# Optimization experiments

Measured on AMD Instinct MI355X. Metric: run time of the kernel, lower is better.

The kernel has to match this reference:

```python
import jax, jax.numpy as jnp
import numpy as np

H = 1024          # hidden_dim
E = 8             # num_experts
TOP_K = 2
FF = 4 * H        # ExpertFFN inner dim (standard transformer FFN assumption)
B, S = 2, 2048


def setup_inputs() -> dict:
    key = jax.random.key(0)
    ks = jax.random.split(key, 12)
    std = 0.02 / np.sqrt(H)
    return {
        "x": jax.random.normal(ks[0], (B, S, H), dtype=jnp.float32),
        "gate_w": jax.random.normal(ks[1], (E, H), dtype=jnp.float32) * std,  # nn.Linear weight [out,in]
        "gate_b": jnp.zeros((E,), dtype=jnp.float32),                          # self.bias param
        # routed experts, stacked: FFN = W2 @ gelu(W1 @ x + b1) + b2
        "w1": jax.random.normal(ks[2], (E, H, FF), dtype=jnp.float32) * (1.0 / np.sqrt(H)),
        "b1": jnp.zeros((E, FF), dtype=jnp.float32),
        "w2": jax.random.normal(ks[3], (E, FF, H), dtype=jnp.float32) * (1.0 / np.sqrt(FF)),
        "b2": jnp.zeros((E, H), dtype=jnp.float32),
        # shared expert
        "sw1": jax.random.normal(ks[4], (H, FF), dtype=jnp.float32) * (1.0 / np.sqrt(H)),
        "sb1": jnp.zeros((FF,), dtype=jnp.float32),
        "sw2": jax.random.normal(ks[5], (FF, H), dtype=jnp.float32) * (1.0 / np.sqrt(FF)),
        "sb2": jnp.zeros((H,), dtype=jnp.float32),
    }


def _moe_forward(x, gate_w, gate_b, w1, b1, w2, b2, sw1, sb1, sw2, sb2):
    b, s, h = x.shape
    xf = x.reshape(-1, h)                                    # [T, H]
    # sigmoid gating with learned bias (aux-loss-free load balancing bias)
    scores = jax.nn.sigmoid(xf @ gate_w.T + gate_b)          # [T, E]
    top_scores, top_idx = jax.lax.top_k(scores, TOP_K)       # [T, k]
    top_scores = top_scores / (top_scores.sum(-1, keepdims=True) + 1e-6)
    # per-expert combine weights: sum of normalized scores over top-k slots
    comb = (jax.nn.one_hot(top_idx, E, dtype=xf.dtype) * top_scores[..., None]).sum(1)  # [T, E]
    # dense grouped FFN over all experts (reference; faithful math to masked dispatch)
    hdn = jax.nn.gelu(jnp.einsum('th,ehf->etf', xf, w1) + b1[:, None, :], approximate=False)
    y = jnp.einsum('etf,efh->eth', hdn, w2) + b2[:, None, :]  # [E, T, H]
    routed = jnp.einsum('te,eth->th', comb, y)                # [T, H]
    shared = (jax.nn.gelu(xf @ sw1 + sb1, approximate=False) @ sw2 + sb2) * 0.1
    return (routed + shared).reshape(b, s, h)                 # dropout: eval mode (identity)


def reference(x, gate_w, gate_b, w1, b1, w2, b2, sw1, sb1, sw2, sb2):
    return _moe_forward(x, gate_w, gate_b, w1, b1, w2, b2, sw1, sb1, sw2, sb2)
```

## Files before the change

kernel.cpp:

```cpp
#include <hip/hip_runtime.h>
#include <stdint.h>

#define H_DIM 1024
#define E_NUM 8
#define FF_DIM 4096
#define T_TOK 4096

typedef __bf16 bf16x8 __attribute__((ext_vector_type(8)));
typedef float f32x4 __attribute__((ext_vector_type(4)));

#define AS1 __attribute__((address_space(1)))
#define AS3 __attribute__((address_space(3)))

__device__ __forceinline__ unsigned short f2bf(float f) {
  union { float f; uint32_t u; } v; v.f = f;
  uint32_t u = v.u;
  uint32_t r = u + 0x7fffu + ((u >> 16) & 1u);
  return (unsigned short)(r >> 16);
}
__device__ __forceinline__ float bf2f(unsigned short u) {
  union { uint32_t u; float f; } v; v.u = ((uint32_t)u) << 16;
  return v.f;
}

__device__ __forceinline__ float gelu_f(float x) {
  float s = x * x;
  float g = x * (1.5957691216f + 0.0713548162f * s);
  float t = __expf(-g);
  return x * __builtin_amdgcn_rcpf(1.0f + t);
}

__global__ __launch_bounds__(64) void gate_kernel(
    const float* __restrict__ x, const float* __restrict__ gw, const float* __restrict__ gb,
    int* __restrict__ topidx, float* __restrict__ topw, int* __restrict__ counts) {
  int t = blockIdx.x;
  int l = threadIdx.x;
  const float* xt = x + (size_t)t * H_DIM;
  float acc[E_NUM];
  #pragma unroll
  for (int e = 0; e < E_NUM; e++) acc[e] = 0.f;
  for (int k = l; k < H_DIM; k += 64) {
    float xv = xt[k];
    #pragma unroll
    for (int e = 0; e < E_NUM; e++) acc[e] += xv * gw[e * H_DIM + k];
  }
  #pragma unroll
  for (int e = 0; e < E_NUM; e++) {
    float v = acc[e];
    #pragma unroll
    for (int off = 32; off > 0; off >>= 1) v += __shfl_xor(v, off, 64);
    acc[e] = v;
  }
  if (l == 0) {
    float s[E_NUM];
    #pragma unroll
    for (int e = 0; e < E_NUM; e++) s[e] = 1.f / (1.f + __expf(-(acc[e] + gb[e])));
    int i1 = 0; float v1 = s[0];
    #pragma unroll
    for (int e = 1; e < E_NUM; e++) if (s[e] > v1) { v1 = s[e]; i1 = e; }
    int i2 = -1; float v2 = -1.f;
    #pragma unroll
    for (int e = 0; e < E_NUM; e++) if (e != i1 && s[e] > v2) { v2 = s[e]; i2 = e; }
    float denom = v1 + v2 + 1e-6f;
    topidx[t * 2]     = i1; topidx[t * 2 + 1] = i2;
    topw[t * 2]       = v1 / denom;
    topw[t * 2 + 1]   = v2 / denom;
    atomicAdd(&counts[i1], 1);
    atomicAdd(&counts[i2], 1);
  }
}

__global__ void init_kernel(int* counts) {
  if (threadIdx.x < E_NUM) counts[threadIdx.x] = 0;
}

__global__ void scan_kernel(const int* __restrict__ counts, int* __restrict__ offs,
                            int* __restrict__ cursor) {
  if (threadIdx.x == 0) {
    int a = 0;
    for (int e = 0; e < E_NUM; e++) { offs[e] = a; a += counts[e]; cursor[e] = 0; }
    offs[E_NUM] = a;
    offs[E_NUM + 1] = a + T_TOK;
  }
}

__global__ void dispatch_kernel(const int* __restrict__ topidx, const float* __restrict__ topw,
                                const int* __restrict__ offs, int* __restrict__ cursor,
                                int* __restrict__ gidx, int* __restrict__ slot_of) {
  int t = blockIdx.x * blockDim.x + threadIdx.x;
  if (t >= T_TOK) return;
  #pragma unroll
  for (int j = 0; j < 2; j++) {
    int ex  = topidx[t * 2 + j];
    int pos = atomicAdd(&cursor[ex], 1);
    int slot = offs[ex] + pos;
    gidx[slot] = t;
    slot_of[t * 2 + j] = slot;
  }
  gidx[2 * T_TOK + t] = t;
}

__global__ __launch_bounds__(256) void gather_x_kernel(
    const float* __restrict__ x, const int* __restrict__ gidx,
    unsigned short* __restrict__ xg) {
  int slot = blockIdx.x;
  int g = threadIdx.x;
  int tok = gidx[slot];
  float4 v = *(const float4*)(x + (size_t)tok * H_DIM + g * 4);
  ushort4 o;
  o.x = f2bf(v.x); o.y = f2bf(v.y); o.z = f2bf(v.z); o.w = f2bf(v.w);
  *(ushort4*)(xg + (size_t)slot * H_DIM + g * 4) = o;
}

__global__ __launch_bounds__(256) void transpose_cast9_kernel(
    const float* __restrict__ w, const float* __restrict__ sw,
    unsigned short* __restrict__ out, int R, int C) {
  __shared__ float tile[64][65];
  const int z = blockIdx.z;
  const float* inb = (z < E_NUM) ? (w + (size_t)z * R * C) : sw;
  unsigned short* outb = out + (size_t)z * R * C;
  int c0 = blockIdx.x * 64, r0 = blockIdx.y * 64;
  int tx = threadIdx.x & 15, ty = threadIdx.x >> 4;
  #pragma unroll
  for (int i = 0; i < 4; i++) {
    int row = ty + i * 16;
    float4 v = *(const float4*)(inb + (size_t)(r0 + row) * C + c0 + tx * 4);
    tile[row][tx * 4 + 0] = v.x;
    tile[row][tx * 4 + 1] = v.y;
    tile[row][tx * 4 + 2] = v.z;
    tile[row][tx * 4 + 3] = v.w;
  }
  __syncthreads();
  int rr0 = tx * 4;
  #pragma unroll
  for (int p = 0; p < 4; p++) {
    int col = p * 16 + ty;
    ushort4 o;
    o.x = f2bf(tile[rr0 + 0][col]);
    o.y = f2bf(tile[rr0 + 1][col]);
    o.z = f2bf(tile[rr0 + 2][col]);
    o.w = f2bf(tile[rr0 + 3][col]);
    *(ushort4*)(outb + (size_t)(c0 + col) * R + r0 + rr0) = o;
  }
}

template <bool FFN1>
__global__ __launch_bounds__(256, 4) void gemm64x256(
    const unsigned short* __restrict__ A,
    const unsigned short* __restrict__ Bt,
    const float* __restrict__ b_r,
    const float* __restrict__ b_s,
    unsigned short* __restrict__ outp,
    const int* __restrict__ offs,
    int K, int N) {
  const int e  = blockIdx.z;
  const int m0 = blockIdx.y * 64;
  const int cnt = offs[e + 1] - offs[e];
  if (m0 >= cnt) return;
  const int base  = offs[e] + m0;
  const int valid = min(64, cnt - m0);
  const int n0 = blockIdx.x * 256;

  __shared__ __align__(16) char ldsA[64 * 128];
  __shared__ __align__(16) char ldsB[256 * 128];

  const int tid = threadIdx.x;
  const int l = tid & 63;

  const int srow = tid >> 3;
  const int su   = (tid & 7) ^ (srow & 7);
  const unsigned short* aSrc[2];
  const unsigned short* bSrc[8];
  const unsigned short* BtE = Bt + (size_t)e * (size_t)N * (size_t)K;
  #pragma unroll
  for (int j = 0; j < 2; j++)
    aSrc[j] = A + (size_t)(base + j * 32 + srow) * (size_t)K + su * 8;
  #pragma unroll
  for (int j = 0; j < 8; j++) {
    int r = j * 32 + srow;
    int rr = r & 63;
    int nr = n0 + (r & 192) + ((rr & 15) << 2) + (rr >> 4);
    bSrc[j] = BtE + (size_t)nr * (size_t)K + su * 8;
  }

  f32x4 acc[4][4];
  #pragma unroll
  for (int m = 0; m < 4; m++)
    #pragma unroll
    for (int n = 0; n < 4; n++) acc[m][n] = (f32x4){0.f, 0.f, 0.f, 0.f};

  const int wc = tid >> 6;
  const int l15 = l & 15, l4 = l >> 4, l7 = l & 7;

  for (int kt = 0; kt < K; kt += 64) {
    #pragma unroll
    for (int j = 0; j < 2; j++)
      __builtin_amdgcn_global_load_lds((const AS1 void*)(aSrc[j] + kt),
                                       (AS3 void*)(ldsA + (j * 256 + tid) * 16), 16, 0, 0);
    #pragma unroll
    for (int j = 0; j < 8; j++)
      __builtin_amdgcn_global_load_lds((const AS1 void*)(bSrc[j] + kt),
                                       (AS3 void*)(ldsB + (j * 256 + tid) * 16), 16, 0, 0);
    __syncthreads();
    #pragma unroll
    for (int kk = 0; kk < 2; kk++) {
      const int uoff = ((kk * 4 + l4) ^ l7) << 4;
      bf16x8 af[4], bfr[4];
      #pragma unroll
      for (int m = 0; m < 4; m++)
        af[m] = *(const bf16x8*)(ldsA + (m * 16 + l15) * 128 + uoff);
      #pragma unroll
      for (int n = 0; n < 4; n++)
        bfr[n] = *(const bf16x8*)(ldsB + (wc * 64 + n * 16 + l15) * 128 + uoff);
      #pragma unroll
      for (int m = 0; m < 4; m++)
        #pragma unroll
        for (int n = 0; n < 4; n++)
          acc[m][n] = __builtin_amdgcn_mfma_f32_16x16x32_bf16(af[m], bfr[n], acc[m][n], 0, 0, 0);
    }
    __syncthreads();
  }

  const float* bias = (e < E_NUM) ? (b_r + (size_t)e * N) : b_s;
  const int c0 = n0 + wc * 64 + 4 * l15;
  float4 bv = *(const float4*)(bias + c0);
  #pragma unroll
  for (int m = 0; m < 4; m++) {
    #pragma unroll
    for (int j = 0; j < 4; j++) {
      int rl = m * 16 + l4 * 4 + j;
      if (rl < valid) {
        ushort4 o;
        if (FFN1) {
          o.x = f2bf(gelu_f(acc[m][0][j] + bv.x));
          o.y = f2bf(gelu_f(acc[m][1][j] + bv.y));
          o.z = f2bf(gelu_f(acc[m][2][j] + bv.z));
          o.w = f2bf(gelu_f(acc[m][3][j] + bv.w));
        } else {
          o.x = f2bf(acc[m][0][j] + bv.x);
          o.y = f2bf(acc[m][1][j] + bv.y);
          o.z = f2bf(acc[m][2][j] + bv.z);
          o.w = f2bf(acc[m][3][j] + bv.w);
        }
        *(ushort4*)(outp + (size_t)(base + rl) * N + c0) = o;
      }
    }
  }
}

__global__ __launch_bounds__(256) void combine_kernel(
    const unsigned short* __restrict__ y, const float* __restrict__ topw,
    const int* __restrict__ slot_of, float* __restrict__ out) {
  int t = blockIdx.x;
  int g = threadIdx.x;
  int s1 = slot_of[2 * t], s2 = slot_of[2 * t + 1];
  float w1 = topw[2 * t], w2 = topw[2 * t + 1];
  ushort4 a = *(const ushort4*)(y + (size_t)s1 * H_DIM + g * 4);
  ushort4 b = *(const ushort4*)(y + (size_t)s2 * H_DIM + g * 4);
  ushort4 c = *(const ushort4*)(y + (size_t)(2 * T_TOK + t) * H_DIM + g * 4);
  float4 o;
  o.x = w1 * bf2f(a.x) + w2 * bf2f(b.x) + 0.1f * bf2f(c.x);
  o.y = w1 * bf2f(a.y) + w2 * bf2f(b.y) + 0.1f * bf2f(c.y);
  o.z = w1 * bf2f(a.z) + w2 * bf2f(b.z) + 0.1f * bf2f(c.z);
  o.w = w1 * bf2f(a.w) + w2 * bf2f(b.w) + 0.1f * bf2f(c.w);
  *(float4*)(out + (size_t)t * H_DIM + g * 4) = o;
}

extern "C" void kernel_launch(void* const* d_in, const int* in_sizes, int n_in,
                              void* d_out, int out_size, void* d_ws, size_t ws_size,
                              hipStream_t stream) {
  const float* x   = (const float*)d_in[0];
  const float* gw  = (const float*)d_in[1];
  const float* gb  = (const float*)d_in[2];
  const float* w1  = (const float*)d_in[3];
  const float* b1  = (const float*)d_in[4];
  const float* w2  = (const float*)d_in[5];
  const float* b2  = (const float*)d_in[6];
  const float* sw1 = (const float*)d_in[7];
  const float* sb1 = (const float*)d_in[8];
  const float* sw2 = (const float*)d_in[9];
  const float* sb2 = (const float*)d_in[10];
  float* out = (float*)d_out;

  char* p = (char*)d_ws;
  auto alloc = [&](size_t bytes) {
    char* r = p;
    p += (bytes + 255) & ~(size_t)255;
    return r;
  };
  int*   counts  = (int*)alloc(E_NUM * 4);
  int*   cursor  = (int*)alloc(E_NUM * 4);
  int*   offs    = (int*)alloc((E_NUM + 2) * 4);
  int*   topidx  = (int*)alloc((size_t)T_TOK * 2 * 4);
  float* topw    = (float*)alloc((size_t)T_TOK * 2 * 4);
  int*   slot_of = (int*)alloc((size_t)T_TOK * 2 * 4);
  int*   gidx    = (int*)alloc((size_t)3 * T_TOK * 4);
  unsigned short* xg   = (unsigned short*)alloc((size_t)3 * T_TOK * H_DIM * 2);
  unsigned short* wAll = (unsigned short*)alloc((size_t)(E_NUM + 1) * FF_DIM * H_DIM * 2);
  unsigned short* hdn  = (unsigned short*)alloc((size_t)3 * T_TOK * FF_DIM * 2);
  unsigned short* yb   = (unsigned short*)alloc((size_t)3 * T_TOK * H_DIM * 2);

  init_kernel<<<1, 64, 0, stream>>>(counts);
  gate_kernel<<<T_TOK, 64, 0, stream>>>(x, gw, gb, topidx, topw, counts);
  scan_kernel<<<1, 1, 0, stream>>>(counts, offs, cursor);
  dispatch_kernel<<<T_TOK / 256, 256, 0, stream>>>(topidx, topw, offs, cursor, gidx, slot_of);

  gather_x_kernel<<<3 * T_TOK, 256, 0, stream>>>(x, gidx, xg);

  transpose_cast9_kernel<<<dim3(FF_DIM / 64, H_DIM / 64, E_NUM + 1), 256, 0, stream>>>(
      w1, sw1, wAll, H_DIM, FF_DIM);
  gemm64x256<true><<<dim3(FF_DIM / 256, T_TOK / 64, E_NUM + 1), 256, 0, stream>>>(
      xg, wAll, b1, sb1, hdn, offs, H_DIM, FF_DIM);

  transpose_cast9_kernel<<<dim3(H_DIM / 64, FF_DIM / 64, E_NUM + 1), 256, 0, stream>>>(
      w2, sw2, wAll, FF_DIM, H_DIM);
  gemm64x256<false><<<dim3(H_DIM / 256, T_TOK / 64, E_NUM + 1), 256, 0, stream>>>(
      hdn, wAll, b2, sb2, yb, offs, FF_DIM, H_DIM);

  combine_kernel<<<T_TOK, 256, 0, stream>>>(yb, topw, slot_of, out);
}
```

Baseline: 545.8 us.

## Double-buffer LDS tiles in grouped GEMM to overlap loads with MFMA

Doubles the LDS buffers for the A and B tiles and prefetches the next K-tile via global_load_lds while MFMAs consume the current one. This leaves one barrier per iteration instead of two, and global latency is meant to hide behind compute. LDS per block doubles to 80KB, so launch bounds drop from 4 to 2 blocks per CU, which lowers occupancy.

```diff
diff --git a/kernel.cpp b/kernel.cpp
--- a/kernel.cpp
+++ b/kernel.cpp
@@ -145,7 +145,7 @@
 }
 
 template <bool FFN1>
-__global__ __launch_bounds__(256, 4) void gemm64x256(
+__global__ __launch_bounds__(256, 2) void gemm64x256(
     const unsigned short* __restrict__ A,
     const unsigned short* __restrict__ Bt,
     const float* __restrict__ b_r,
@@ -161,8 +161,8 @@
   const int valid = min(64, cnt - m0);
   const int n0 = blockIdx.x * 256;
 
-  __shared__ __align__(16) char ldsA[64 * 128];
-  __shared__ __align__(16) char ldsB[256 * 128];
+  __shared__ __align__(16) char ldsA[2][64 * 128];
+  __shared__ __align__(16) char ldsB[2][256 * 128];
 
   const int tid = threadIdx.x;
   const int l = tid & 63;
@@ -183,6 +183,18 @@
     bSrc[j] = BtE + (size_t)nr * (size_t)K + su * 8;
   }
 
+#define STAGE(c, kt)                                                                \
+  {                                                                                 \
+    _Pragma("unroll")                                                               \
+    for (int j = 0; j < 2; j++)                                                     \
+      __builtin_amdgcn_global_load_lds((const AS1 void*)(aSrc[j] + (kt) * 64),      \
+          (AS3 void*)(&ldsA[c][(j * 256 + tid) * 16]), 16, 0, 0);                   \
+    _Pragma("unroll")                                                               \
+    for (int j = 0; j < 8; j++)                                                     \
+      __builtin_amdgcn_global_load_lds((const AS1 void*)(bSrc[j] + (kt) * 64),      \
+          (AS3 void*)(&ldsB[c][(j * 256 + tid) * 16]), 16, 0, 0);                   \
+  }
+
   f32x4 acc[4][4];
   #pragma unroll
   for (int m = 0; m < 4; m++)
@@ -191,27 +203,27 @@
 
   const int wc = tid >> 6;
   const int l15 = l & 15, l4 = l >> 4, l7 = l & 7;
-
-  for (int kt = 0; kt < K; kt += 64) {
-    #pragma unroll
-    for (int j = 0; j < 2; j++)
-      __builtin_amdgcn_global_load_lds((const AS1 void*)(aSrc[j] + kt),
-                                       (AS3 void*)(ldsA + (j * 256 + tid) * 16), 16, 0, 0);
-    #pragma unroll
-    for (int j = 0; j < 8; j++)
-      __builtin_amdgcn_global_load_lds((const AS1 void*)(bSrc[j] + kt),
-                                       (AS3 void*)(ldsB + (j * 256 + tid) * 16), 16, 0, 0);
-    __syncthreads();
+  const int nt = K >> 6;
+
+  STAGE(0, 0);
+  __syncthreads();
+
+  for (int t = 0; t < nt; t++) {
+    const int cur = t & 1;
+    if (t + 1 < nt) STAGE(cur ^ 1, t + 1);
+
+    const char* pA = &ldsA[cur][0];
+    const char* pB = &ldsB[cur][0];
     #pragma unroll
     for (int kk = 0; kk < 2; kk++) {
       const int uoff = ((kk * 4 + l4) ^ l7) << 4;
       bf16x8 af[4], bfr[4];
       #pragma unroll
       for (int m = 0; m < 4; m++)
-        af[m] = *(const bf16x8*)(ldsA + (m * 16 + l15) * 128 + uoff);
+        af[m] = *(const bf16x8*)(pA + (m * 16 + l15) * 128 + uoff);
       #pragma unroll
       for (int n = 0; n < 4; n++)
-        bfr[n] = *(const bf16x8*)(ldsB + (wc * 64 + n * 16 + l15) * 128 + uoff);
+        bfr[n] = *(const bf16x8*)(pB + (wc * 64 + n * 16 + l15) * 128 + uoff);
       #pragma unroll
       for (int m = 0; m < 4; m++)
         #pragma unroll
@@ -220,6 +232,7 @@
     }
     __syncthreads();
   }
+#undef STAGE
 
   const float* bias = (e < E_NUM) ? (b_r + (size_t)e * N) : b_s;
   const int c0 = n0 + wc * 64 + 4 * l15;
```

Measured after the change: 616.3 us. 12.9% more time.

## Overlap W2 transpose-cast with the first expert GEMM via extra grid slice

Applied to the files above, without the earlier changes.

The separate launch that transposes and casts W2 to bf16 is folded into the FFN1 GEMM launch as an extra blockIdx.z slice. Those blocks transpose the W2 and shared-W2 tiles into a second weight buffer while the other blocks compute FFN1. This removes one kernel launch and lets the memory-bound transpose run alongside the compute-bound GEMM. The cost is a second weight workspace, and the transpose blocks now run at the GEMM's launch bounds and LDS layout, with each block looping over 9 matrices serially.

```diff
diff --git a/kernel.cpp b/kernel.cpp
--- a/kernel.cpp
+++ b/kernel.cpp
@@ -152,7 +152,47 @@
     const float* __restrict__ b_s,
     unsigned short* __restrict__ outp,
     const int* __restrict__ offs,
+    const float* __restrict__ w2src,
+    const float* __restrict__ sw2src,
+    unsigned short* __restrict__ w2t,
     int K, int N) {
+  __shared__ __align__(16) char ldsA[64 * 128];
+  __shared__ __align__(16) char ldsB[256 * 128];
+
+  if (FFN1 && blockIdx.z == E_NUM + 1) {
+    float (*tile)[65] = (float (*)[65])ldsB;
+    const int c0 = blockIdx.x * 64;
+    const int r0 = blockIdx.y * 64;
+    const int tx = threadIdx.x & 15, ty = threadIdx.x >> 4;
+    for (int z2 = 0; z2 <= E_NUM; z2++) {
+      const float* inb = (z2 < E_NUM) ? (w2src + (size_t)z2 * FF_DIM * H_DIM) : sw2src;
+      unsigned short* outb = w2t + (size_t)z2 * FF_DIM * H_DIM;
+      #pragma unroll
+      for (int i = 0; i < 4; i++) {
+        int row = ty + i * 16;
+        float4 v = *(const float4*)(inb + (size_t)(r0 + row) * H_DIM + c0 + tx * 4);
+        tile[row][tx * 4 + 0] = v.x;
+        tile[row][tx * 4 + 1] = v.y;
+        tile[row][tx * 4 + 2] = v.z;
+        tile[row][tx * 4 + 3] = v.w;
+      }
+      __syncthreads();
+      int rr0 = tx * 4;
+      #pragma unroll
+      for (int p = 0; p < 4; p++) {
+        int col = p * 16 + ty;
+        ushort4 o;
+        o.x = f2bf(tile[rr0 + 0][col]);
+        o.y = f2bf(tile[rr0 + 1][col]);
+        o.z = f2bf(tile[rr0 + 2][col]);
+        o.w = f2bf(tile[rr0 + 3][col]);
+        *(ushort4*)(outb + (size_t)(c0 + col) * FF_DIM + r0 + rr0) = o;
+      }
+      __syncthreads();
+    }
+    return;
+  }
+
   const int e  = blockIdx.z;
   const int m0 = blockIdx.y * 64;
   const int cnt = offs[e + 1] - offs[e];
@@ -160,9 +200,6 @@
   const int base  = offs[e] + m0;
   const int valid = min(64, cnt - m0);
   const int n0 = blockIdx.x * 256;
-
-  __shared__ __align__(16) char ldsA[64 * 128];
-  __shared__ __align__(16) char ldsB[256 * 128];
 
   const int tid = threadIdx.x;
   const int l = tid & 63;
@@ -295,10 +332,11 @@
   float* topw    = (float*)alloc((size_t)T_TOK * 2 * 4);
   int*   slot_of = (int*)alloc((size_t)T_TOK * 2 * 4);
   int*   gidx    = (int*)alloc((size_t)3 * T_TOK * 4);
-  unsigned short* xg   = (unsigned short*)alloc((size_t)3 * T_TOK * H_DIM * 2);
-  unsigned short* wAll = (unsigned short*)alloc((size_t)(E_NUM + 1) * FF_DIM * H_DIM * 2);
-  unsigned short* hdn  = (unsigned short*)alloc((size_t)3 * T_TOK * FF_DIM * 2);
-  unsigned short* yb   = (unsigned short*)alloc((size_t)3 * T_TOK * H_DIM * 2);
+  unsigned short* xg    = (unsigned short*)alloc((size_t)3 * T_TOK * H_DIM * 2);
+  unsigned short* wAll1 = (unsigned short*)alloc((size_t)(E_NUM + 1) * FF_DIM * H_DIM * 2);
+  unsigned short* wAll2 = (unsigned short*)alloc((size_t)(E_NUM + 1) * FF_DIM * H_DIM * 2);
+  unsigned short* hdn   = (unsigned short*)alloc((size_t)3 * T_TOK * FF_DIM * 2);
+  unsigned short* yb    = (unsigned short*)alloc((size_t)3 * T_TOK * H_DIM * 2);
 
   init_kernel<<<1, 64, 0, stream>>>(counts);
   gate_kernel<<<T_TOK, 64, 0, stream>>>(x, gw, gb, topidx, topw, counts);
@@ -308,14 +346,13 @@
   gather_x_kernel<<<3 * T_TOK, 256, 0, stream>>>(x, gidx, xg);
 
   transpose_cast9_kernel<<<dim3(FF_DIM / 64, H_DIM / 64, E_NUM + 1), 256, 0, stream>>>(
-      w1, sw1, wAll, H_DIM, FF_DIM);
-  gemm64x256<true><<<dim3(FF_DIM / 256, T_TOK / 64, E_NUM + 1), 256, 0, stream>>>(
-      xg, wAll, b1, sb1, hdn, offs, H_DIM, FF_DIM);
-
-  transpose_cast9_kernel<<<dim3(H_DIM / 64, FF_DIM / 64, E_NUM + 1), 256, 0, stream>>>(
-      w2, sw2, wAll, FF_DIM, H_DIM);
+      w1, sw1, wAll1, H_DIM, FF_DIM);
+
+  gemm64x256<true><<<dim3(FF_DIM / 256, T_TOK / 64, E_NUM + 2), 256, 0, stream>>>(
+      xg, wAll1, b1, sb1, hdn, offs, w2, sw2, wAll2, H_DIM, FF_DIM);
+
   gemm64x256<false><<<dim3(H_DIM / 256, T_TOK / 64, E_NUM + 1), 256, 0, stream>>>(
-      hdn, wAll, b2, sb2, yb, offs, FF_DIM, H_DIM);
+      hdn, wAll2, b2, sb2, yb, offs, nullptr, nullptr, nullptr, FF_DIM, H_DIM);
 
   combine_kernel<<<T_TOK, 256, 0, stream>>>(yb, topw, slot_of, out);
 }
```

After: 535.1 us, median of 2. No clear change (-2.0%).
